# Performance work log

Measured on AMD Instinct MI355X. Metric: run time of the kernel, lower is better.

## Reference

```python
import jax, jax.numpy as jnp
import numpy as np

EMB = 256
HEADS = 4
HD = EMB // HEADS
BS, SZ = 4, 64


def _layernorm(x, g, b, eps=1e-5):
    mu = jnp.mean(x, axis=-1, keepdims=True)
    var = jnp.mean((x - mu) ** 2, axis=-1, keepdims=True)
    return (x - mu) * jax.lax.rsqrt(var + eps) * g + b


def setup_inputs() -> dict:
    key = jax.random.key(0)
    ks = jax.random.split(key, 12)
    s = lambda k, shape, sc: jax.random.normal(k, shape, jnp.float32) * sc
    return {
        "x": s(ks[0], (BS, EMB, SZ, SZ), 1.0),
        "ln1_g": jnp.ones((EMB,), jnp.float32),
        "ln1_b": jnp.zeros((EMB,), jnp.float32),
        "wq": s(ks[1], (HD, HD), HD ** -0.5), "bq": jnp.zeros((HD,), jnp.float32),
        "wk": s(ks[2], (HD, HD), HD ** -0.5), "bk": jnp.zeros((HD,), jnp.float32),
        "wv": s(ks[3], (HD, HD), HD ** -0.5), "bv": jnp.zeros((HD,), jnp.float32),
        "wo": s(ks[4], (EMB, EMB), EMB ** -0.5), "bo": jnp.zeros((EMB,), jnp.float32),
        "ln2_g": jnp.ones((EMB,), jnp.float32),
        "ln2_b": jnp.zeros((EMB,), jnp.float32),
        "w1": s(ks[5], (EMB, EMB), EMB ** -0.5), "b1": jnp.zeros((EMB,), jnp.float32),
        "w2": s(ks[6], (EMB, EMB), EMB ** -0.5), "b2": jnp.zeros((EMB,), jnp.float32),
    }


def reference(x, ln1_g, ln1_b, wq, bq, wk, bk, wv, bv, wo, bo, ln2_g, ln2_b, w1, b1, w2, b2):
    bs, c, sz, _ = x.shape
    seq = sz * sz
    xt = x.reshape(bs, c, seq).swapaxes(1, 2)  # [b, s, c]
    xn = _layernorm(xt, ln1_g, ln1_b)
    # split heads: [b, h, s, d]
    h = xn.reshape(bs, seq, HEADS, HD).transpose(0, 2, 1, 3)
    q = h @ wq + bq
    k = h @ wk + bk
    v = h @ wv + bv
    scores = jnp.einsum("bhqd,bhkd->bhqk", q, k) / (HD ** 0.5)
    attn = jax.nn.softmax(scores, axis=-1)
    o = jnp.einsum("bhqk,bhkd->bhqd", attn, v)
    o = o.transpose(0, 2, 1, 3).reshape(bs, seq, c)
    o = o @ wo + bo
    av = o + xt  # residual 1
    ff = _layernorm(av, ln2_g, ln2_b) @ w1 + b1
    ff = jax.nn.gelu(ff, approximate=False) @ w2 + b2
    out = ff + av  # residual 2
    return out.swapaxes(1, 2).reshape(bs, c, sz, sz)
```

## Files before the change

kernel.cpp:

```cpp
#include <hip/hip_runtime.h>
#include <hip/hip_bf16.h>
#include <cstdint>

typedef __attribute__((ext_vector_type(8))) short short8;
typedef __attribute__((ext_vector_type(4))) short short4_;
typedef __attribute__((ext_vector_type(4))) float float4_;
typedef __attribute__((ext_vector_type(16))) float f32x16;

#define MFMA16(a,b,c)  __builtin_amdgcn_mfma_f32_16x16x32_bf16(a,b,c,0,0,0)
#define MFMA32(a,b,c)  __builtin_amdgcn_mfma_f32_32x32x16_bf16(a,b,c,0,0,0)
#define EXP2(x) __builtin_amdgcn_exp2f(x)

__device__ __forceinline__ short f2bs(float f) {
    union { float f; uint32_t u; } c;
    c.f = f;
    c.u += 0x7FFF + ((c.u >> 16) & 1);
    return (short)(c.u >> 16);
}
__device__ __forceinline__ float s2f(short s) {
    union { uint32_t u; float f; } c;
    c.u = ((uint32_t)(uint16_t)s) << 16;
    return c.f;
}

static const int EMB = 256;
static const int SEQ = 4096;
static const int TOK = 16384;

static const size_t SZO = 4194304;
static const size_t LSTRIDE = 65536;

#define QSCALE 0.18033688011112042f

__global__ __launch_bounds__(256) void repack_kernel(
    const float* wq, const float* wk, const float* wv,
    const float* wo, const float* w1, const float* w2,
    short* wqT, short* wkT, short* wvT, short* woT, short* w1T, short* w2T)
{
    int idx = blockIdx.x * 256 + threadIdx.x;
    if (idx < 3 * 4096) {
        int m = idx / 4096, r = idx % 4096;
        int n = r / 64, k = r % 64;
        const float* src = (m == 0) ? wq : (m == 1) ? wk : wv;
        short* dst = (m == 0) ? wqT : (m == 1) ? wkT : wvT;
        float v = src[k * 64 + n];
        if (m == 0) v *= QSCALE;
        dst[n * 64 + k] = f2bs(v);
    } else {
        int idx2 = idx - 3 * 4096;
        if (idx2 < 3 * 65536) {
            int m = idx2 / 65536, r = idx2 % 65536;
            int n = r / 256, k = r % 256;
            const float* src = (m == 0) ? wo : (m == 1) ? w1 : w2;
            short* dst = (m == 0) ? woT : (m == 1) ? w1T : w2T;
            dst[n * 256 + k] = f2bs(src[k * 256 + n]);
        }
    }
}

__global__ __launch_bounds__(512, 2) void ln1qkv_kernel(
    const float* x, const float* g, const float* bta,
    const short* wqT, const short* wkT, const short* wvT,
    const float* bq, const float* bk, const float* bv,
    short* xt, short* qo, short* ko, short* vto)
{
    __shared__ short xn_lds[64 * 264];
    __shared__ float redS[8][64], redQ[8][64];

    int tid = threadIdx.x;
    int l = tid & 63;
    int cp = tid >> 6;
    int t = blockIdx.x * 64 + l;
    int b = t >> 12, sp = t & 4095;
    const float* xb = x + (size_t)b * EMB * SEQ + (size_t)(cp * 32) * SEQ + sp;

    float v[32];
#pragma unroll
    for (int j = 0; j < 32; j++) v[j] = xb[(size_t)j * SEQ];
    float sum = 0.f, ss = 0.f;
#pragma unroll
    for (int j = 0; j < 32; j++) { sum += v[j]; ss += v[j] * v[j]; }
    redS[cp][l] = sum;
    redQ[cp][l] = ss;
    __syncthreads();
    float S = 0.f, Q = 0.f;
#pragma unroll
    for (int p = 0; p < 8; p++) { S += redS[p][l]; Q += redQ[p][l]; }
    float mu = S * (1.f / 256.f);
    float var = Q * (1.f / 256.f) - mu * mu;
    float rs = rsqrtf(var + 1e-5f);

    short* xtr = xt + (size_t)t * 256 + cp * 32;
    short* xnr = xn_lds + l * 264 + cp * 32;
#pragma unroll
    for (int c = 0; c < 32; c += 8) {
        short8 ra, na;
#pragma unroll
        for (int j = 0; j < 8; j++) {
            float vv = v[c + j];
            ra[j] = f2bs(vv);
            na[j] = f2bs((vv - mu) * rs * g[cp * 32 + c + j] + bta[cp * 32 + c + j]);
        }
        *(short8*)(xtr + c) = ra;
        *(short8*)(xnr + c) = na;
    }
    __syncthreads();

    int w = tid >> 6;
    int lane = tid & 63, quad = lane >> 4, l15 = lane & 15;
    int tt = w >> 1;
    int odd = w & 1;
    int m0 = blockIdx.x * 64 + tt * 16;
    int row = m0 + l15;
    int bb = row >> 12;

    const short* arow = xn_lds + (tt * 16 + l15) * 264;
    short8 a0[4], a1[4];
#pragma unroll
    for (int h = 0; h < 4; h++) {
        a0[h] = *(const short8*)(arow + h * 64 + quad * 8);
        a1[h] = *(const short8*)(arow + h * 64 + 32 + quad * 8);
    }

    {
        const short* WT = odd ? wkT : wqT;
        const float* bias = odd ? bk : bq;
        float bscale = odd ? 1.f : QSCALE;
        short* dst = odd ? ko : qo;
        int s0 = (m0 & 4095) + quad * 4;
#pragma unroll
        for (int nb = 0; nb < 4; nb++) {
            int col = nb * 16 + l15;
            short8 b0 = *(const short8*)(WT + col * 64 + quad * 8);
            short8 b1 = *(const short8*)(WT + col * 64 + 32 + quad * 8);
            float bvv = bias[col] * bscale;
#pragma unroll
            for (int h = 0; h < 4; h++) {
                float4_ acc = {bvv, bvv, bvv, bvv};
                acc = MFMA16(a0[h], b0, acc);
                acc = MFMA16(a1[h], b1, acc);
                size_t headbase = (size_t)(bb * 4 + h) * SEQ;
#pragma unroll
                for (int r = 0; r < 4; r++)
                    dst[(headbase + s0 + r) * 64 + col] = f2bs(acc[r]);
            }
        }
    }

    {
        int sp0 = m0 & 4095;
#pragma unroll
        for (int nbi = 0; nbi < 2; nbi++) {
            int nb = odd * 2 + nbi;
            int colw = nb * 16 + l15;
            short8 b0 = *(const short8*)(wvT + colw * 64 + quad * 8);
            short8 b1 = *(const short8*)(wvT + colw * 64 + 32 + quad * 8);
            float4_ binit;
#pragma unroll
            for (int r = 0; r < 4; r++) binit[r] = bv[nb * 16 + quad * 4 + r];
#pragma unroll
            for (int h = 0; h < 4; h++) {
                float4_ acc = binit;
                acc = MFMA16(b0, a0[h], acc);
                acc = MFMA16(b1, a1[h], acc);
                size_t dbase = ((size_t)(bb * 4 + h) * 64 + nb * 16 + quad * 4) * SEQ;
#pragma unroll
                for (int r = 0; r < 4; r++)
                    vto[dbase + (size_t)r * SEQ + sp0 + l15] = f2bs(acc[r]);
            }
        }
    }
}

__global__ __attribute__((amdgpu_flat_work_group_size(256, 256),
                          amdgpu_waves_per_eu(2, 4)))
void flash_kernel(
    const short* q, const short* k, const short* vt,
    short* O0, short* Orest, float* lbase)
{
    __shared__ short K_lds[128 * 64];
    __shared__ short V_lds[64 * 128];

    int tid = threadIdx.x;
    int w = tid >> 6, lane = tid & 63;
    int l31 = lane & 31, hh = lane >> 5;
    int qt = blockIdx.x, bh = blockIdx.y, grp = blockIdx.z;
    int span = 64 / gridDim.z;
    int nst = span >> 1;

    const short* qb = q + (size_t)bh * SEQ * 64;
    const short* kb = k + (size_t)bh * SEQ * 64 + (size_t)grp * span * 64 * 64;
    const short* vb = vt + (size_t)bh * 64 * SEQ + grp * span * 64;

    int qrow = qt * 128 + w * 32 + l31;
    short8 qf[4];
#pragma unroll
    for (int kb4 = 0; kb4 < 4; kb4++)
        qf[kb4] = *(const short8*)(qb + (size_t)qrow * 64 + kb4 * 16 + hh * 8);

    f32x16 oacc[2];
#pragma unroll
    for (int td = 0; td < 2; td++)
#pragma unroll
        for (int i = 0; i < 16; i++) oacc[td][i] = 0.f;
    float li = 0.f;

    int srow = tid >> 2;
    int c0 = tid & 3;
    int sw = (srow & 7) ^ ((srow & 1) << 2);
    int rw = (l31 & 7) ^ ((l31 & 1) << 2);

    int dcA = (c0 ^ sw) << 3;
    int dcB = ((c0 + 4) ^ sw) << 3;

    short8 kr0 = *(const short8*)(kb + (size_t)srow * 64 + c0 * 8);
    short8 kr1 = *(const short8*)(kb + (size_t)srow * 64 + (c0 + 4) * 8);
    short8 kr2 = *(const short8*)(kb + (size_t)(64 + srow) * 64 + c0 * 8);
    short8 kr3 = *(const short8*)(kb + (size_t)(64 + srow) * 64 + (c0 + 4) * 8);
    short8 vr0 = *(const short8*)(vb + (size_t)srow * SEQ + c0 * 8);
    short8 vr1 = *(const short8*)(vb + (size_t)srow * SEQ + (c0 + 4) * 8);
    short8 vr2 = *(const short8*)(vb + (size_t)srow * SEQ + 64 + c0 * 8);
    short8 vr3 = *(const short8*)(vb + (size_t)srow * SEQ + 64 + (c0 + 4) * 8);

    for (int st = 0; st < nst; st++) {
        __syncthreads();
        *(short8*)&K_lds[srow * 64 + dcA] = kr0;
        *(short8*)&K_lds[srow * 64 + dcB] = kr1;
        *(short8*)&K_lds[(64 + srow) * 64 + dcA] = kr2;
        *(short8*)&K_lds[(64 + srow) * 64 + dcB] = kr3;
        *(short8*)&V_lds[srow * 128 + dcA] = vr0;
        *(short8*)&V_lds[srow * 128 + dcB] = vr1;
        *(short8*)&V_lds[srow * 128 + 64 + dcA] = vr2;
        *(short8*)&V_lds[srow * 128 + 64 + dcB] = vr3;
        if (st + 1 < nst) {
            size_t ko = (size_t)((st + 1) * 128 + srow) * 64;
            kr0 = *(const short8*)(kb + ko + c0 * 8);
            kr1 = *(const short8*)(kb + ko + (c0 + 4) * 8);
            kr2 = *(const short8*)(kb + ko + 64 * 64 + c0 * 8);
            kr3 = *(const short8*)(kb + ko + 64 * 64 + (c0 + 4) * 8);
            size_t vo = (size_t)srow * SEQ + (st + 1) * 128;
            vr0 = *(const short8*)(vb + vo + c0 * 8);
            vr1 = *(const short8*)(vb + vo + (c0 + 4) * 8);
            vr2 = *(const short8*)(vb + vo + 64 + c0 * 8);
            vr3 = *(const short8*)(vb + vo + 64 + (c0 + 4) * 8);
        }
        asm volatile("s_waitcnt lgkmcnt(0)" ::: "memory");
        __builtin_amdgcn_s_barrier();
        asm volatile("" ::: "memory");

#pragma unroll
        for (int t = 0; t < 4; t++) {
            f32x16 acc;
#pragma unroll
            for (int i = 0; i < 16; i++) acc[i] = 0.f;
#pragma unroll
            for (int kb4 = 0; kb4 < 4; kb4++) {
                short8 ka = *(const short8*)&K_lds[(t * 32 + l31) * 64 +
                                                   (((kb4 * 2 + hh) ^ rw) << 3)];
                acc = MFMA32(ka, qf[kb4], acc);
            }
#pragma unroll
            for (int i = 0; i < 16; i++) acc[i] = EXP2(acc[i]);
            li += ((acc[0] + acc[1]) + (acc[2] + acc[3]))
                + ((acc[4] + acc[5]) + (acc[6] + acc[7]))
                + ((acc[8] + acc[9]) + (acc[10] + acc[11]))
                + ((acc[12] + acc[13]) + (acc[14] + acc[15]));
            short8 wf[2];
#pragma unroll
            for (int kbl = 0; kbl < 2; kbl++) {
                uint32_t A0, A1, B0, B1;
                asm("v_cvt_pk_bf16_f32 %0, %1, %2" : "=v"(A0)
                    : "v"(acc[kbl * 8 + 0]), "v"(acc[kbl * 8 + 1]));
                asm("v_cvt_pk_bf16_f32 %0, %1, %2" : "=v"(A1)
                    : "v"(acc[kbl * 8 + 2]), "v"(acc[kbl * 8 + 3]));
                asm("v_cvt_pk_bf16_f32 %0, %1, %2" : "=v"(B0)
                    : "v"(acc[kbl * 8 + 4]), "v"(acc[kbl * 8 + 5]));
                asm("v_cvt_pk_bf16_f32 %0, %1, %2" : "=v"(B1)
                    : "v"(acc[kbl * 8 + 6]), "v"(acc[kbl * 8 + 7]));
                asm("v_permlane32_swap_b32 %0, %1" : "+v"(A0), "+v"(B0));
                asm("v_permlane32_swap_b32 %0, %1" : "+v"(A1), "+v"(B1));
                union { short8 s; uint32_t u[4]; } pw;
                pw.u[0] = A0; pw.u[1] = A1; pw.u[2] = B0; pw.u[3] = B1;
                wf[kbl] = pw.s;
            }
            __builtin_amdgcn_s_setprio(1);
#pragma unroll
            for (int kbl = 0; kbl < 2; kbl++) {
                int kc = (t * 2 + kbl) * 2 + hh;
                int kcs = (kc & 8) | ((kc & 7) ^ rw);
#pragma unroll
                for (int td = 0; td < 2; td++) {
                    short8 va = *(const short8*)&V_lds[(td * 32 + l31) * 128 +
                                                       (kcs << 3)];
                    oacc[td] = MFMA32(va, wf[kbl], oacc[td]);
                }
            }
            __builtin_amdgcn_s_setprio(0);
        }
    }

    li += __shfl_xor(li, 32);

    short* Op = grp ? (Orest + (size_t)(grp - 1) * SZO) : O0;
    float* lp = lbase + (size_t)grp * LSTRIDE;
    if (hh == 0) lp[bh * 4096 + qrow] = li;

    size_t ob = ((size_t)bh * 4096 + qrow) * 64;
#pragma unroll
    for (int td = 0; td < 2; td++)
#pragma unroll
        for (int g = 0; g < 4; g++) {
            short4_ pk;
#pragma unroll
            for (int r = 0; r < 4; r++) pk[r] = f2bs(oacc[td][g * 4 + r]);
            *(short4_*)(Op + ob + td * 32 + g * 8 + hh * 4) = pk;
        }
}

__global__ __launch_bounds__(256) void combine_kernel(
    const short* O0, const short* Orest, const float* lb,
    short* Oout, int np)
{
    int g = blockIdx.x * 256 + threadIdx.x;
    int qi = g >> 4;
    short4_ a = *(const short4_*)(O0 + (size_t)g * 4);
    float l = lb[qi];
    float4_ acc = {s2f(a[0]), s2f(a[1]), s2f(a[2]), s2f(a[3])};
    for (int j = 1; j < np; j++) {
        short4_ b = *(const short4_*)(Orest + (size_t)(j - 1) * SZO + (size_t)g * 4);
        l += lb[(size_t)j * LSTRIDE + qi];
#pragma unroll
        for (int jj = 0; jj < 4; jj++) acc[jj] += s2f(b[jj]);
    }
    float inv = 1.f / l;
    short4_ pk;
#pragma unroll
    for (int j = 0; j < 4; j++) pk[j] = f2bs(acc[j] * inv);
    *(short4_*)(Oout + (size_t)g * 4) = pk;
}

__global__ __launch_bounds__(512, 2) void mlp_kernel(
    const short* O0, const short* Orest, const float* lb, int np,
    const short* woT, const short* w1T, const short* w2T,
    const float* bo, const float* b1, const float* b2,
    const float* g2, const float* be2,
    const short* xt, float* outf)
{
    __shared__ __align__(16) char smem[3 * 16896 + 256];
    short* av = (short*)smem;
    short* x2 = (short*)(smem + 16896);
    short* ff = (short*)(smem + 33792);
    float* stats = (float*)(smem + 50688);
    float* T = (float*)smem;

    int tid = threadIdx.x;
    int w = tid >> 6, lane = tid & 63, quad = lane >> 4, l15 = lane & 15;
    int m0 = blockIdx.x * 32;
    int th = w >> 2;
    int n0 = (w & 3) * 64;
    int arow = m0 + th * 16 + l15;
    int bbA = arow >> 12, spA = arow & 4095;

    float invh[4];
    if (np) {
#pragma unroll
        for (int h = 0; h < 4; h++) {
            size_t li = (size_t)(bbA * 4 + h) * 4096 + spA;
            float s = lb[li];
            for (int j = 1; j < np; j++) s += lb[(size_t)j * LSTRIDE + li];
            invh[h] = 1.f / s;
        }
    }

    float4_ acc[4];
#pragma unroll
    for (int nb = 0; nb < 4; nb++) {
        float bvv = bo[n0 + nb * 16 + l15];
        acc[nb] = {bvv, bvv, bvv, bvv};
    }
    for (int kc = 0; kc < 8; kc++) {
        int h = kc >> 1;
        int off = (kc & 1) * 32 + quad * 8;
        size_t obase = ((size_t)(bbA * 4 + h) * 4096 + spA) * 64 + off;
        short8 a;
        if (np) {
            short8 a0v = *(const short8*)(O0 + obase);
            float f[8];
#pragma unroll
            for (int jj = 0; jj < 8; jj++) f[jj] = s2f(a0v[jj]);
            for (int j = 1; j < np; j++) {
                short8 apv = *(const short8*)(Orest + (size_t)(j - 1) * SZO + obase);
#pragma unroll
                for (int jj = 0; jj < 8; jj++) f[jj] += s2f(apv[jj]);
            }
            float iv = invh[h];
            union { short8 s; uint32_t u[4]; } pa;
#pragma unroll
            for (int jj = 0; jj < 4; jj++) {
                float f0 = f[2 * jj] * iv;
                float f1 = f[2 * jj + 1] * iv;
                asm("v_cvt_pk_bf16_f32 %0, %1, %2" : "=v"(pa.u[jj]) : "v"(f0), "v"(f1));
            }
            a = pa.s;
        } else {
            a = *(const short8*)(O0 + obase);
        }
#pragma unroll
        for (int nb = 0; nb < 4; nb++) {
            short8 b = *(const short8*)(woT + (size_t)(n0 + nb * 16 + l15) * 256 + kc * 32 + quad * 8);
            acc[nb] = MFMA16(a, b, acc[nb]);
        }
    }
#pragma unroll
    for (int nb = 0; nb < 4; nb++) {
        int col = n0 + nb * 16 + l15;
#pragma unroll
        for (int r = 0; r < 4; r++) {
            size_t t = (size_t)m0 + th * 16 + quad * 4 + r;
            av[(th * 16 + quad * 4 + r) * 264 + col] = f2bs(acc[nb][r] + s2f(xt[t * 256 + col]));
        }
    }
    __syncthreads();

    {
        int row = tid >> 4, sub = tid & 15;
        float sum = 0.f, ss = 0.f;
        short8 v0 = *(const short8*)&av[row * 264 + sub * 16];
        short8 v1 = *(const short8*)&av[row * 264 + sub * 16 + 8];
#pragma unroll
        for (int j = 0; j < 8; j++) {
            float a = s2f(v0[j]), b = s2f(v1[j]);
            sum += a + b; ss += a * a + b * b;
        }
#pragma unroll
        for (int off = 1; off < 16; off <<= 1) {
            sum += __shfl_xor(sum, off);
            ss += __shfl_xor(ss, off);
        }
        if (sub == 0) {
            float mu = sum * (1.f / 256.f);
            float var = ss * (1.f / 256.f) - mu * mu;
            stats[row] = mu;
            stats[32 + row] = rsqrtf(var + 1e-5f);
        }
    }
    __syncthreads();

    {
        int row = tid >> 4, sub = tid & 15;
        float mu = stats[row], rs = stats[32 + row];
#pragma unroll
        for (int j = 0; j < 16; j += 4) {
            int c = sub * 16 + j;
            short4_ rv = *(const short4_*)&av[row * 264 + c];
            short4_ pk;
#pragma unroll
            for (int i = 0; i < 4; i++)
                pk[i] = f2bs((s2f(rv[i]) - mu) * rs * g2[c + i] + be2[c + i]);
            *(short4_*)&x2[row * 264 + c] = pk;
        }
    }
    __syncthreads();

#pragma unroll
    for (int nb = 0; nb < 4; nb++) {
        float bvv = b1[n0 + nb * 16 + l15];
        acc[nb] = {bvv, bvv, bvv, bvv};
    }
    for (int kc = 0; kc < 8; kc++) {
        short8 a = *(const short8*)&x2[(th * 16 + l15) * 264 + kc * 32 + quad * 8];
#pragma unroll
        for (int nb = 0; nb < 4; nb++) {
            short8 b = *(const short8*)(w1T + (size_t)(n0 + nb * 16 + l15) * 256 + kc * 32 + quad * 8);
            acc[nb] = MFMA16(a, b, acc[nb]);
        }
    }
#pragma unroll
    for (int nb = 0; nb < 4; nb++) {
        int col = n0 + nb * 16 + l15;
#pragma unroll
        for (int r = 0; r < 4; r++) {
            float v = acc[nb][r];
            v = 0.5f * v * (1.f + erff(v * 0.70710678118f));
            ff[(th * 16 + quad * 4 + r) * 264 + col] = f2bs(v);
        }
    }
    __syncthreads();

#pragma unroll
    for (int nb = 0; nb < 4; nb++) {
        float bvv = b2[n0 + nb * 16 + l15];
        acc[nb] = {bvv, bvv, bvv, bvv};
    }
    for (int kc = 0; kc < 8; kc++) {
        short8 a = *(const short8*)&ff[(th * 16 + l15) * 264 + kc * 32 + quad * 8];
#pragma unroll
        for (int nb = 0; nb < 4; nb++) {
            short8 b = *(const short8*)(w2T + (size_t)(n0 + nb * 16 + l15) * 256 + kc * 32 + quad * 8);
            acc[nb] = MFMA16(a, b, acc[nb]);
        }
    }
    float vout[4][4];
#pragma unroll
    for (int nb = 0; nb < 4; nb++) {
        int col = n0 + nb * 16 + l15;
#pragma unroll
        for (int r = 0; r < 4; r++)
            vout[nb][r] = acc[nb][r] + s2f(av[(th * 16 + quad * 4 + r) * 264 + col]);
    }
    __syncthreads();

    float* tw = T + w * 1040;
#pragma unroll
    for (int nb = 0; nb < 4; nb++)
#pragma unroll
        for (int r = 0; r < 4; r++)
            tw[(quad * 4 + r) * 65 + nb * 16 + l15] = vout[nb][r];

    int bb = m0 >> 12;
    int spb = (m0 & 4095) + th * 16;
    float* dst = outf + ((size_t)bb * 256 + n0 + lane) * SEQ + spb;
#pragma unroll
    for (int j = 0; j < 16; j += 4) {
        float4_ pk = {tw[(j + 0) * 65 + lane], tw[(j + 1) * 65 + lane],
                      tw[(j + 2) * 65 + lane], tw[(j + 3) * 65 + lane]};
        *(float4_*)(dst + j) = pk;
    }
}

extern "C" void kernel_launch(void* const* d_in, const int* in_sizes, int n_in,
                              void* d_out, int out_size, void* d_ws, size_t ws_size,
                              hipStream_t stream)
{
    const float* x     = (const float*)d_in[0];
    const float* ln1_g = (const float*)d_in[1];
    const float* ln1_b = (const float*)d_in[2];
    const float* wq    = (const float*)d_in[3];
    const float* bq    = (const float*)d_in[4];
    const float* wk    = (const float*)d_in[5];
    const float* bk    = (const float*)d_in[6];
    const float* wv    = (const float*)d_in[7];
    const float* bv    = (const float*)d_in[8];
    const float* wo    = (const float*)d_in[9];
    const float* bo    = (const float*)d_in[10];
    const float* ln2_g = (const float*)d_in[11];
    const float* ln2_b = (const float*)d_in[12];
    const float* w1    = (const float*)d_in[13];
    const float* b1    = (const float*)d_in[14];
    const float* w2    = (const float*)d_in[15];
    const float* b2    = (const float*)d_in[16];

    char* ws = (char*)d_ws;
    const size_t SZ_BF = (size_t)TOK * 256 * 2;

    short* wqT = (short*)(ws + 0);
    short* wkT = (short*)(ws + 8192);
    short* wvT = (short*)(ws + 16384);
    short* woT = (short*)(ws + 24576);
    short* w1T = (short*)(ws + 155648);
    short* w2T = (short*)(ws + 286720);
    char* base = ws + 524288;

    short* xt  = (short*)(base);
    short* kbuf= (short*)(base + SZ_BF);
    short* vtb = (short*)(base + 2 * SZ_BF);

    const size_t need2_fb = 524288 + 3 * SZ_BF + 524288 + SZ_BF;
    const size_t need2_fu = need2_fb + SZ_BF;

    int nz, fuse;
    if (ws_size >= need2_fu)      { nz = 2; fuse = 1; }
    else if (ws_size >= need2_fb) { nz = 2; fuse = 0; }
    else                          { nz = 1; fuse = 0; }

    float* lbase = (float*)(base + 3 * SZ_BF);
    short* Orest = (short*)(base + 3 * SZ_BF + 524288);
    short* O0w   = Orest + SZO;

    short* qb  = (short*)d_out;
    short* upper = (short*)((char*)d_out + SZ_BF);
    short* O0  = fuse ? O0w : upper;
    short* Onrm= vtb;

    repack_kernel<<<816, 256, 0, stream>>>(wq, wk, wv, wo, w1, w2,
                                           wqT, wkT, wvT, woT, w1T, w2T);
    ln1qkv_kernel<<<TOK / 64, 512, 0, stream>>>(x, ln1_g, ln1_b,
                                                wqT, wkT, wvT, bq, bk, bv,
                                                xt, qb, kbuf, vtb);
    flash_kernel<<<dim3(32, 16, nz), 256, 0, stream>>>(qb, kbuf, vtb, O0, Orest, lbase);
    if (fuse) {
        mlp_kernel<<<TOK / 32, 512, 0, stream>>>(O0, Orest, lbase, nz,
                                                 woT, w1T, w2T, bo, b1, b2,
                                                 ln2_g, ln2_b, xt, (float*)d_out);
    } else {
        combine_kernel<<<4096, 256, 0, stream>>>(O0, Orest, lbase, Onrm, nz);
        mlp_kernel<<<TOK / 32, 512, 0, stream>>>(Onrm, Orest, lbase, 0,
                                                 woT, w1T, w2T, bo, b1, b2,
                                                 ln2_g, ln2_b, xt, (float*)d_out);
    }
}
```

Before: 251.2 us.

## Double flash-attention block to 512 threads covering 256 query rows

The flash attention kernel now runs 8 waves per block, covering 256 query rows instead of 128. Each shared K/V tile loaded into LDS is reused by twice as many query rows, and each thread loads half as many vectors per stage. The grid's query dimension is halved, which leaves fewer blocks (16x16xnz) to fill the GPU. The larger block also risks lower occupancy and costlier barriers.

```diff
diff --git a/kernel.cpp b/kernel.cpp
--- a/kernel.cpp
+++ b/kernel.cpp
@@ -172,7 +172,7 @@
     }
 }
 
-__global__ __attribute__((amdgpu_flat_work_group_size(256, 256),
+__global__ __attribute__((amdgpu_flat_work_group_size(512, 512),
                           amdgpu_waves_per_eu(2, 4)))
 void flash_kernel(
     const short* q, const short* k, const short* vt,
@@ -192,7 +192,7 @@
     const short* kb = k + (size_t)bh * SEQ * 64 + (size_t)grp * span * 64 * 64;
     const short* vb = vt + (size_t)bh * 64 * SEQ + grp * span * 64;
 
-    int qrow = qt * 128 + w * 32 + l31;
+    int qrow = qt * 256 + w * 32 + l31;
     short8 qf[4];
 #pragma unroll
     for (int kb4 = 0; kb4 < 4; kb4++)
@@ -205,44 +205,33 @@
         for (int i = 0; i < 16; i++) oacc[td][i] = 0.f;
     float li = 0.f;
 
-    int srow = tid >> 2;
-    int c0 = tid & 3;
+    int srow = tid >> 3;
+    int c0 = tid & 7;
     int sw = (srow & 7) ^ ((srow & 1) << 2);
     int rw = (l31 & 7) ^ ((l31 & 1) << 2);
 
-    int dcA = (c0 ^ sw) << 3;
-    int dcB = ((c0 + 4) ^ sw) << 3;
+    int dcK = (c0 ^ sw) << 3;
+    int dcV0 = (c0 ^ sw) << 3;
+    int dcV1 = (8 | (c0 ^ sw)) << 3;
 
     short8 kr0 = *(const short8*)(kb + (size_t)srow * 64 + c0 * 8);
-    short8 kr1 = *(const short8*)(kb + (size_t)srow * 64 + (c0 + 4) * 8);
-    short8 kr2 = *(const short8*)(kb + (size_t)(64 + srow) * 64 + c0 * 8);
-    short8 kr3 = *(const short8*)(kb + (size_t)(64 + srow) * 64 + (c0 + 4) * 8);
+    short8 kr1 = *(const short8*)(kb + (size_t)(64 + srow) * 64 + c0 * 8);
     short8 vr0 = *(const short8*)(vb + (size_t)srow * SEQ + c0 * 8);
-    short8 vr1 = *(const short8*)(vb + (size_t)srow * SEQ + (c0 + 4) * 8);
-    short8 vr2 = *(const short8*)(vb + (size_t)srow * SEQ + 64 + c0 * 8);
-    short8 vr3 = *(const short8*)(vb + (size_t)srow * SEQ + 64 + (c0 + 4) * 8);
+    short8 vr1 = *(const short8*)(vb + (size_t)srow * SEQ + 64 + c0 * 8);
 
     for (int st = 0; st < nst; st++) {
         __syncthreads();
-        *(short8*)&K_lds[srow * 64 + dcA] = kr0;
-        *(short8*)&K_lds[srow * 64 + dcB] = kr1;
-        *(short8*)&K_lds[(64 + srow) * 64 + dcA] = kr2;
-        *(short8*)&K_lds[(64 + srow) * 64 + dcB] = kr3;
-        *(short8*)&V_lds[srow * 128 + dcA] = vr0;
-        *(short8*)&V_lds[srow * 128 + dcB] = vr1;
-        *(short8*)&V_lds[srow * 128 + 64 + dcA] = vr2;
-        *(short8*)&V_lds[srow * 128 + 64 + dcB] = vr3;
+        *(short8*)&K_lds[srow * 64 + dcK] = kr0;
+        *(short8*)&K_lds[(64 + srow) * 64 + dcK] = kr1;
+        *(short8*)&V_lds[srow * 128 + dcV0] = vr0;
+        *(short8*)&V_lds[srow * 128 + dcV1] = vr1;
         if (st + 1 < nst) {
             size_t ko = (size_t)((st + 1) * 128 + srow) * 64;
             kr0 = *(const short8*)(kb + ko + c0 * 8);
-            kr1 = *(const short8*)(kb + ko + (c0 + 4) * 8);
-            kr2 = *(const short8*)(kb + ko + 64 * 64 + c0 * 8);
-            kr3 = *(const short8*)(kb + ko + 64 * 64 + (c0 + 4) * 8);
+            kr1 = *(const short8*)(kb + ko + 64 * 64 + c0 * 8);
             size_t vo = (size_t)srow * SEQ + (st + 1) * 128;
             vr0 = *(const short8*)(vb + vo + c0 * 8);
-            vr1 = *(const short8*)(vb + vo + (c0 + 4) * 8);
-            vr2 = *(const short8*)(vb + vo + 64 + c0 * 8);
-            vr3 = *(const short8*)(vb + vo + 64 + (c0 + 4) * 8);
+            vr1 = *(const short8*)(vb + vo + 64 + c0 * 8);
         }
         asm volatile("s_waitcnt lgkmcnt(0)" ::: "memory");
         __builtin_amdgcn_s_barrier();
@@ -587,7 +576,7 @@
     ln1qkv_kernel<<<TOK / 64, 512, 0, stream>>>(x, ln1_g, ln1_b,
                                                 wqT, wkT, wvT, bq, bk, bv,
                                                 xt, qb, kbuf, vtb);
-    flash_kernel<<<dim3(32, 16, nz), 256, 0, stream>>>(qb, kbuf, vtb, O0, Orest, lbase);
+    flash_kernel<<<dim3(16, 16, nz), 512, 0, stream>>>(qb, kbuf, vtb, O0, Orest, lbase);
     if (fuse) {
         mlp_kernel<<<TOK / 32, 512, 0, stream>>>(O0, Orest, lbase, nz,
                                                  woT, w1T, w2T, bo, b1, b2,
```

Measured after the change: 247.4 us. No clear change (-1.5%).
